# Kernel tuning notes

Measured on AMD Instinct MI355X. Metric: run time of the kernel, lower is better.

## Reference

```python
import jax, jax.numpy as jnp
import numpy as np

D_MODEL = 1024
NUM_HEADS = 16
D_K = D_MODEL // NUM_HEADS


def setup_inputs() -> dict:
    key = jax.random.key(0)
    ks = jax.random.split(key, 9)
    B, T = 2, 2048
    s = 1.0 / np.sqrt(D_MODEL)
    return {
        "x": jax.random.normal(ks[0], (B, T, D_MODEL), dtype=jnp.float32),
        "w_q": jax.random.normal(ks[1], (D_MODEL, D_MODEL), dtype=jnp.float32) * s,
        "b_q": jnp.zeros((D_MODEL,), dtype=jnp.float32),
        "w_k": jax.random.normal(ks[2], (D_MODEL, D_MODEL), dtype=jnp.float32) * s,
        "b_k": jnp.zeros((D_MODEL,), dtype=jnp.float32),
        "w_v": jax.random.normal(ks[3], (D_MODEL, D_MODEL), dtype=jnp.float32) * s,
        "b_v": jnp.zeros((D_MODEL,), dtype=jnp.float32),
        "w_o": jax.random.normal(ks[4], (D_MODEL, D_MODEL), dtype=jnp.float32) * s,
        "b_o": jnp.zeros((D_MODEL,), dtype=jnp.float32),
    }


def reference(x, w_q, b_q, w_k, b_k, w_v, b_v, w_o, b_o):
    B, T, D = x.shape
    H, dk = NUM_HEADS, D_K

    def proj(w, b):
        # [B,T,D] -> [B,H,T,dk]; Linear uses y = x @ W^T + b
        y = jnp.einsum("btd,ed->bte", x, w) + b
        return y.reshape(B, T, H, dk).transpose(0, 2, 1, 3)

    q = proj(w_q, b_q)
    k = proj(w_k, b_k)
    v = proj(w_v, b_v)

    scores = jnp.einsum("bhtd,bhsd->bhts", q, k) / jnp.sqrt(jnp.float32(dk))
    attn = jax.nn.softmax(scores, axis=-1)  # dropout is identity in eval
    out = jnp.einsum("bhts,bhsd->bhtd", attn, v)
    out = out.transpose(0, 2, 1, 3).reshape(B, T, D)
    return jnp.einsum("btd,ed->bte", out, w_o) + b_o
```

## Files before the change

### kernel.cpp

```cpp
#include <hip/hip_runtime.h>

typedef __bf16 bf16x8 __attribute__((ext_vector_type(8)));
typedef float f32x4 __attribute__((ext_vector_type(4)));
typedef float f32x16 __attribute__((ext_vector_type(16)));

__device__ __forceinline__ unsigned short f2bf(float f) {
    unsigned u = __builtin_bit_cast(unsigned, f);
    u += 0x7FFFu + ((u >> 16) & 1u);
    return (unsigned short)(u >> 16);
}
__device__ __forceinline__ float bf2f(unsigned short u) {
    return __builtin_bit_cast(float, (unsigned)u << 16);
}
__device__ __forceinline__ unsigned cvtpk_bf16(float lo, float hi) {
    unsigned r;
    asm("v_cvt_pk_bf16_f32 %0, %1, %2" : "=v"(r) : "v"(lo), "v"(hi));
    return r;
}
__device__ __forceinline__ float exp2_hw(float x) {
    float r;
    asm("v_exp_f32 %0, %1" : "=v"(r) : "v"(x));
    return r;
}

__device__ __forceinline__ void gload16(const void* g, void* l) {
    __builtin_amdgcn_global_load_lds(
        (const __attribute__((address_space(1))) void*)g,
        (__attribute__((address_space(3))) void*)l, 16, 0, 0);
}

__global__ __launch_bounds__(256) void cvt_all(const float* __restrict__ x,
    const float* __restrict__ w0, const float* __restrict__ w1,
    const float* __restrict__ w2, const float* __restrict__ w3,
    unsigned short* __restrict__ xb, unsigned short* __restrict__ wout)
{
    int i = blockIdx.x * 256 + threadIdx.x;
    const float* src;
    unsigned short* dst;
    int j;
    if (i < 1048576) {
        src = x; dst = xb; j = i;
    } else {
        int k = i - 1048576;
        int m = k >> 18;
        src = (m == 0) ? w0 : (m == 1) ? w1 : (m == 2) ? w2 : w3;
        dst = wout + (size_t)m * 1048576;
        j = k & 262143;
    }
    float4 v = reinterpret_cast<const float4*>(src)[j];
    ushort4 o;
    o.x = f2bf(v.x); o.y = f2bf(v.y); o.z = f2bf(v.z); o.w = f2bf(v.w);
    reinterpret_cast<ushort4*>(dst)[j] = o;
}

__global__ __launch_bounds__(256) void qkv_gemm(const unsigned short* __restrict__ X,
    const unsigned short* __restrict__ Wqkv,
    const float* __restrict__ bq, const float* __restrict__ bk, const float* __restrict__ bv,
    unsigned short* __restrict__ Qb, unsigned short* __restrict__ Kb, unsigned short* __restrict__ Vt)
{
    __shared__ __align__(16) unsigned short sA[128 * 64];
    __shared__ __align__(16) unsigned short sW[64 * 64];
    f32x4 acc[4][2] = {};
    const int id = blockIdx.x;
    const int xcd = id & 7, local = id >> 3;
    const int m = (xcd & 1) * 16 + (local & 15);
    const int n = (xcd >> 1) * 12 + (local >> 4);
    const int m0 = m * 128, n0 = n * 64;

    const int tid  = threadIdx.x;
    const int lane = tid & 63;
    const int wv   = tid >> 6;
    const int wm   = wv >> 1, wn = wv & 1;
    const int lrow = lane >> 3;
    const int lchunk = (lane & 7) ^ lrow;

    char* sAc = reinterpret_cast<char*>(sA);
    char* sWc = reinterpret_cast<char*>(sW);

    for (int kt = 0; kt < 1024; kt += 64) {
        __syncthreads();
        #pragma unroll
        for (int j = 0; j < 4; ++j) {
            int row = (wv * 4 + j) * 8 + lrow;
            gload16(X + (size_t)(m0 + row) * 1024 + kt + lchunk * 8, sAc + (wv * 4 + j) * 1024);
        }
        #pragma unroll
        for (int j = 0; j < 2; ++j) {
            int row = (wv * 2 + j) * 8 + lrow;
            gload16(Wqkv + (size_t)(n0 + row) * 1024 + kt + lchunk * 8, sWc + (wv * 2 + j) * 1024);
        }
        __syncthreads();
        #pragma unroll
        for (int kk = 0; kk < 2; ++kk) {
            bf16x8 af[4], wf[2];
            #pragma unroll
            for (int r = 0; r < 4; ++r) {
                int rowA = wm * 64 + r * 16 + (lane & 15);
                int ca = ((kk * 4 + (lane >> 4)) ^ (rowA & 7)) * 16;
                af[r] = *reinterpret_cast<const bf16x8*>(sAc + rowA * 128 + ca);
            }
            #pragma unroll
            for (int c = 0; c < 2; ++c) {
                int rowW = wn * 32 + c * 16 + (lane & 15);
                int cw = ((kk * 4 + (lane >> 4)) ^ (rowW & 7)) * 16;
                wf[c] = *reinterpret_cast<const bf16x8*>(sWc + rowW * 128 + cw);
            }
            #pragma unroll
            for (int r = 0; r < 4; ++r)
                #pragma unroll
                for (int c = 0; c < 2; ++c)
                    acc[r][c] = __builtin_amdgcn_mfma_f32_16x16x32_bf16(af[r], wf[c], acc[r][c], 0, 0, 0);
        }
    }

    const int mid = n0 >> 10;
    const float* bias = (mid == 0) ? bq : (mid == 1) ? bk : bv;
    const float qs = (mid == 0) ? 0.18033688011112042f : 1.0f;
    #pragma unroll
    for (int r = 0; r < 4; ++r) {
        #pragma unroll
        for (int c = 0; c < 2; ++c) {
            int colg = n0 + wn * 32 + c * 16 + (lane & 15);
            int col = colg & 1023;
            float bb = bias[col];
            int row0 = m0 + wm * 64 + r * 16 + 4 * (lane >> 4);
            if (mid == 2) {
                ushort4 sv;
                sv.x = f2bf(acc[r][c][0] + bb);
                sv.y = f2bf(acc[r][c][1] + bb);
                sv.z = f2bf(acc[r][c][2] + bb);
                sv.w = f2bf(acc[r][c][3] + bb);
                *reinterpret_cast<ushort4*>(
                    Vt + ((size_t)((row0 >> 11) * 1024 + col)) * 2048 + (row0 & 2047)) = sv;
            } else {
                #pragma unroll
                for (int e = 0; e < 4; ++e) {
                    unsigned short bf = f2bf((acc[r][c][e] + bb) * qs);
                    if (mid == 0) Qb[(size_t)(row0 + e) * 1024 + col] = bf;
                    else          Kb[(size_t)(row0 + e) * 1024 + col] = bf;
                }
            }
        }
    }
}

__global__ __launch_bounds__(256) void out_gemm(const unsigned short* __restrict__ O,
    const unsigned short* __restrict__ Wo, const float* __restrict__ bo,
    float* __restrict__ out)
{
    __shared__ __align__(16) unsigned short sA[128 * 64];
    __shared__ __align__(16) unsigned short sW[64 * 64];
    f32x4 acc[4][2] = {};
    const int m0 = blockIdx.x * 128, n0 = blockIdx.y * 64;

    const int tid  = threadIdx.x;
    const int lane = tid & 63;
    const int wv   = tid >> 6;
    const int wm   = wv >> 1, wn = wv & 1;
    const int lrow = lane >> 3;
    const int lchunk = (lane & 7) ^ lrow;

    char* sAc = reinterpret_cast<char*>(sA);
    char* sWc = reinterpret_cast<char*>(sW);

    for (int kt = 0; kt < 1024; kt += 64) {
        __syncthreads();
        #pragma unroll
        for (int j = 0; j < 4; ++j) {
            int row = (wv * 4 + j) * 8 + lrow;
            gload16(O + (size_t)(m0 + row) * 1024 + kt + lchunk * 8, sAc + (wv * 4 + j) * 1024);
        }
        #pragma unroll
        for (int j = 0; j < 2; ++j) {
            int row = (wv * 2 + j) * 8 + lrow;
            gload16(Wo + (size_t)(n0 + row) * 1024 + kt + lchunk * 8, sWc + (wv * 2 + j) * 1024);
        }
        __syncthreads();
        #pragma unroll
        for (int kk = 0; kk < 2; ++kk) {
            bf16x8 af[4], wf[2];
            #pragma unroll
            for (int r = 0; r < 4; ++r) {
                int rowA = wm * 64 + r * 16 + (lane & 15);
                int ca = ((kk * 4 + (lane >> 4)) ^ (rowA & 7)) * 16;
                af[r] = *reinterpret_cast<const bf16x8*>(sAc + rowA * 128 + ca);
            }
            #pragma unroll
            for (int c = 0; c < 2; ++c) {
                int rowW = wn * 32 + c * 16 + (lane & 15);
                int cw = ((kk * 4 + (lane >> 4)) ^ (rowW & 7)) * 16;
                wf[c] = *reinterpret_cast<const bf16x8*>(sWc + rowW * 128 + cw);
            }
            #pragma unroll
            for (int r = 0; r < 4; ++r)
                #pragma unroll
                for (int c = 0; c < 2; ++c)
                    acc[r][c] = __builtin_amdgcn_mfma_f32_16x16x32_bf16(af[r], wf[c], acc[r][c], 0, 0, 0);
        }
    }

    #pragma unroll
    for (int r = 0; r < 4; ++r) {
        #pragma unroll
        for (int c = 0; c < 2; ++c) {
            int col = n0 + wn * 32 + c * 16 + (lane & 15);
            float bb = bo[col];
            #pragma unroll
            for (int e = 0; e < 4; ++e) {
                int row = m0 + wm * 64 + r * 16 + 4 * (lane >> 4) + e;
                out[(size_t)row * 1024 + col] = acc[r][c][e] + bb;
            }
        }
    }
}

__global__ __launch_bounds__(256) void combine_kernel(
    const unsigned short* __restrict__ O0, const unsigned short* __restrict__ O1,
    const float* __restrict__ lbase, unsigned short* __restrict__ Ob)
{
    int idx = blockIdx.x * 256 + threadIdx.x;
    int row = idx >> 7;
    int h = (idx & 127) >> 3;
    float lsum = lbase[row * 16 + h] + lbase[65536 + row * 16 + h];
    float inv = 1.0f / lsum;
    uint4 x0 = reinterpret_cast<const uint4*>(O0)[idx];
    uint4 x1 = reinterpret_cast<const uint4*>(O1)[idx];
    const unsigned* p0 = reinterpret_cast<const unsigned*>(&x0);
    const unsigned* p1 = reinterpret_cast<const unsigned*>(&x1);
    uint4 o;
    unsigned* po = reinterpret_cast<unsigned*>(&o);
    #pragma unroll
    for (int wd = 0; wd < 4; ++wd) {
        float lo = bf2f((unsigned short)(p0[wd] & 0xFFFF)) + bf2f((unsigned short)(p1[wd] & 0xFFFF));
        float hi = bf2f((unsigned short)(p0[wd] >> 16)) + bf2f((unsigned short)(p1[wd] >> 16));
        po[wd] = cvtpk_bf16(lo * inv, hi * inv);
    }
    reinterpret_cast<uint4*>(Ob)[idx] = o;
}

__global__ __launch_bounds__(512) void attn_kernel(const unsigned short* __restrict__ Qb,
    const unsigned short* __restrict__ Kb, const unsigned short* __restrict__ Vt,
    unsigned short* __restrict__ Oq0, unsigned short* __restrict__ Oq1,
    float* __restrict__ lbase)
{
    __shared__ __align__(16) unsigned short sK[2][64 * 64];
    __shared__ __align__(16) unsigned short sV[2][64 * 64];

    const int id = blockIdx.x;
    const int swz = (id & 7) * 64 + (id >> 3);
    const int qt = swz & 7;
    const int bh = (swz >> 3) & 31;
    const int half = swz >> 8;
    const int b = bh >> 4, h = bh & 15;
    const int tid = threadIdx.x, lane = tid & 63, wv = tid >> 6;
    const int qq = lane & 31, hi = lane >> 5;

    unsigned short* Oh = half ? Oq1 : Oq0;
    float* lq = lbase + half * 65536;

    const int qrow0 = b * 2048 + qt * 256 + wv * 32;
    const int kv0 = half * 1024;
    const int ntiles = 16;

    bf16x8 qf[4];
    #pragma unroll
    for (int ks = 0; ks < 4; ++ks)
        qf[ks] = *reinterpret_cast<const bf16x8*>(
            Qb + (size_t)(qrow0 + qq) * 1024 + h * 64 + ks * 16 + hi * 8);

    f32x16 oacc[2] = {};
    float l_sum = 0.f;

    const unsigned short* Kbase = Kb + (size_t)b * 2048 * 1024 + h * 64;
    const unsigned short* Vbase = Vt + (size_t)(bh * 64) * 2048;

    const int lrow = lane >> 3;
    const int lchunk = (lane & 7) ^ lrow;

    char* sKbase = reinterpret_cast<char*>(sK);
    char* sVbase = reinterpret_cast<char*>(sV);

    #define FILL(buf, kvoff)                                                              \
        {                                                                                 \
            int row = wv * 8 + lrow;                                                      \
            gload16(Kbase + (size_t)((kvoff) + row) * 1024 + lchunk * 8,                  \
                    sKbase + (buf) * 8192 + wv * 1024);                                   \
            gload16(Vbase + (size_t)row * 2048 + (kvoff) + lchunk * 8,                    \
                    sVbase + (buf) * 8192 + wv * 1024);                                   \
        }

    FILL(0, kv0)
    __syncthreads();

    for (int t = 0; t < ntiles; ++t) {
        const int cur = t & 1;
        if (t < ntiles - 1) { FILL(cur ^ 1, kv0 + (t + 1) * 64) }

        const char* bK = sKbase + cur * 8192;
        const char* bV = sVbase + cur * 8192;

        f32x16 pacc[2];
        __builtin_amdgcn_s_setprio(1);
        #pragma unroll
        for (int mt = 0; mt < 2; ++mt) {
            f32x16 acc = {};
            int row = mt * 32 + qq;
            #pragma unroll
            for (int ks = 0; ks < 4; ++ks) {
                int c = ((ks * 2 + hi) ^ (row & 7)) * 16;
                bf16x8 kf = *reinterpret_cast<const bf16x8*>(bK + row * 128 + c);
                acc = __builtin_amdgcn_mfma_f32_32x32x16_bf16(kf, qf[ks], acc, 0, 0, 0);
            }
            pacc[mt] = acc;
        }
        __builtin_amdgcn_s_setprio(0);

        float rs0 = 0.f, rs1 = 0.f, rs2 = 0.f, rs3 = 0.f;
        #pragma unroll
        for (int mt = 0; mt < 2; ++mt) {
            #pragma unroll
            for (int r = 0; r < 16; r += 4) {
                float p0 = exp2_hw(pacc[mt][r + 0]);
                float p1 = exp2_hw(pacc[mt][r + 1]);
                float p2 = exp2_hw(pacc[mt][r + 2]);
                float p3 = exp2_hw(pacc[mt][r + 3]);
                pacc[mt][r + 0] = p0; rs0 += p0;
                pacc[mt][r + 1] = p1; rs1 += p1;
                pacc[mt][r + 2] = p2; rs2 += p2;
                pacc[mt][r + 3] = p3; rs3 += p3;
            }
        }
        l_sum += (rs0 + rs1) + (rs2 + rs3);

        __builtin_amdgcn_s_setprio(1);
        #pragma unroll
        for (int mt = 0; mt < 2; ++mt) {
            #pragma unroll
            for (int halfk = 0; halfk < 2; ++halfk) {
                int r0 = halfk * 8;
                unsigned A0 = cvtpk_bf16(pacc[mt][r0 + 0], pacc[mt][r0 + 1]);
                unsigned A1 = cvtpk_bf16(pacc[mt][r0 + 2], pacc[mt][r0 + 3]);
                unsigned B0 = cvtpk_bf16(pacc[mt][r0 + 4], pacc[mt][r0 + 5]);
                unsigned B1 = cvtpk_bf16(pacc[mt][r0 + 6], pacc[mt][r0 + 7]);
                unsigned t0 = hi ? A0 : B0;
                unsigned t1 = hi ? A1 : B1;
                unsigned r0x = (unsigned)__shfl_xor((int)t0, 32);
                unsigned r1x = (unsigned)__shfl_xor((int)t1, 32);
                union { unsigned u[4]; bf16x8 v; } pf;
                pf.u[0] = hi ? r0x : A0;
                pf.u[1] = hi ? r1x : A1;
                pf.u[2] = hi ? B0 : r0x;
                pf.u[3] = hi ? B1 : r1x;
                int ks = mt * 2 + halfk;
                #pragma unroll
                for (int dt = 0; dt < 2; ++dt) {
                    int row = dt * 32 + qq;
                    int c = ((ks * 2 + hi) ^ (row & 7)) * 16;
                    bf16x8 vf = *reinterpret_cast<const bf16x8*>(bV + row * 128 + c);
                    oacc[dt] = __builtin_amdgcn_mfma_f32_32x32x16_bf16(vf, pf.v, oacc[dt], 0, 0, 0);
                }
            }
        }
        __builtin_amdgcn_s_setprio(0);
        __syncthreads();
    }

    #pragma unroll
    for (int dt = 0; dt < 2; ++dt) {
        #pragma unroll
        for (int rg = 0; rg < 4; ++rg) {
            int d0 = dt * 32 + rg * 8 + hi * 4;
            ushort4 stv;
            stv.x = f2bf(oacc[dt][rg * 4 + 0]);
            stv.y = f2bf(oacc[dt][rg * 4 + 1]);
            stv.z = f2bf(oacc[dt][rg * 4 + 2]);
            stv.w = f2bf(oacc[dt][rg * 4 + 3]);
            *reinterpret_cast<ushort4*>(Oh + (size_t)(qrow0 + qq) * 1024 + h * 64 + d0) = stv;
        }
    }
    l_sum = l_sum + __shfl_xor(l_sum, 32);
    if (hi == 0)
        lq[(qrow0 + qq) * 16 + h] = l_sum;
}

extern "C" void kernel_launch(void* const* d_in, const int* in_sizes, int n_in,
                              void* d_out, int out_size, void* d_ws, size_t ws_size,
                              hipStream_t stream)
{
    const float* x  = (const float*)d_in[0];
    const float* wq = (const float*)d_in[1];
    const float* bq = (const float*)d_in[2];
    const float* wk = (const float*)d_in[3];
    const float* bk = (const float*)d_in[4];
    const float* wv = (const float*)d_in[5];
    const float* bv = (const float*)d_in[6];
    const float* wo = (const float*)d_in[7];
    const float* bo = (const float*)d_in[8];
    float* out = (float*)d_out;

    char* ws = (char*)d_ws;
    const size_t MB = 1024 * 1024;
    unsigned short* xb   = (unsigned short*)(ws + 0);
    unsigned short* wqkv = (unsigned short*)(ws + 8 * MB);
    unsigned short* wob  = (unsigned short*)(ws + 14 * MB);
    unsigned short* Qb   = (unsigned short*)(ws + 16 * MB);
    unsigned short* Kb   = (unsigned short*)(ws + 24 * MB);
    unsigned short* Vt   = (unsigned short*)(ws + 32 * MB);
    unsigned short* O0   = (unsigned short*)(ws + 40 * MB);
    unsigned short* O1   = (unsigned short*)(ws + 48 * MB);
    float*          lse0 = (float*)(ws + 56 * MB);
    unsigned short* Ob   = Qb;

    cvt_all<<<8192, 256, 0, stream>>>(x, wq, wk, wv, wo, xb, wqkv);

    qkv_gemm<<<1536, 256, 0, stream>>>(xb, wqkv, bq, bk, bv, Qb, Kb, Vt);
    attn_kernel<<<512, 512, 0, stream>>>(Qb, Kb, Vt, O0, O1, lse0);
    combine_kernel<<<2048, 256, 0, stream>>>(O0, O1, lse0, Ob);
    out_gemm<<<dim3(32, 16), 256, 0, stream>>>(Ob, wob, bo, out);
}
```

Baseline: 114.7 us.

## Software-pipeline QK^T of next tile with softmax and PV of current tile

Restructures the attention loop so the QK^T MFMAs for tile t+1 are issued before the exp/softmax and PV MFMAs of tile t, using two score register buffers and a loop unrolled by two. K loads now run two tiles ahead and V loads one tile ahead, each in separate double buffers. The goal is to overlap the exp work (VALU/transcendental) with matrix work and hide shared-memory latency. It costs another 32 floats of live registers per lane, which may reduce occupancy.

```diff
diff --git a/kernel.cpp b/kernel.cpp
--- a/kernel.cpp
+++ b/kernel.cpp
@@ -260,7 +260,6 @@
 
     const int qrow0 = b * 2048 + qt * 256 + wv * 32;
     const int kv0 = half * 1024;
-    const int ntiles = 16;
 
     bf16x8 qf[4];
     #pragma unroll
@@ -269,6 +268,7 @@
             Qb + (size_t)(qrow0 + qq) * 1024 + h * 64 + ks * 16 + hi * 8);
 
     f32x16 oacc[2] = {};
+    f32x16 pP[2][2];
     float l_sum = 0.f;
 
     const unsigned short* Kbase = Kb + (size_t)b * 2048 * 1024 + h * 64;
@@ -280,89 +280,114 @@
     char* sKbase = reinterpret_cast<char*>(sK);
     char* sVbase = reinterpret_cast<char*>(sV);
 
-    #define FILL(buf, kvoff)                                                              \
-        {                                                                                 \
-            int row = wv * 8 + lrow;                                                      \
-            gload16(Kbase + (size_t)((kvoff) + row) * 1024 + lchunk * 8,                  \
-                    sKbase + (buf) * 8192 + wv * 1024);                                   \
-            gload16(Vbase + (size_t)row * 2048 + (kvoff) + lchunk * 8,                    \
-                    sVbase + (buf) * 8192 + wv * 1024);                                   \
-        }
-
-    FILL(0, kv0)
+    #define FILL_K(buf, kvoff)                                                           \
+        {                                                                                \
+            int row = wv * 8 + lrow;                                                     \
+            gload16(Kbase + (size_t)((kvoff) + row) * 1024 + lchunk * 8,                 \
+                    sKbase + (buf) * 8192 + wv * 1024);                                  \
+        }
+    #define FILL_V(buf, kvoff)                                                           \
+        {                                                                                \
+            int row = wv * 8 + lrow;                                                     \
+            gload16(Vbase + (size_t)row * 2048 + (kvoff) + lchunk * 8,                   \
+                    sVbase + (buf) * 8192 + wv * 1024);                                  \
+        }
+
+    #define QKT(S, tn)                                                                   \
+        {                                                                                \
+            const char* bK = sKbase + ((tn) & 1) * 8192;                                 \
+            __builtin_amdgcn_s_setprio(1);                                               \
+            _Pragma("unroll")                                                            \
+            for (int mt = 0; mt < 2; ++mt) {                                             \
+                f32x16 acc = {};                                                         \
+                int row = mt * 32 + qq;                                                  \
+                _Pragma("unroll")                                                        \
+                for (int ks = 0; ks < 4; ++ks) {                                         \
+                    int c = ((ks * 2 + hi) ^ (row & 7)) * 16;                            \
+                    bf16x8 kf = *reinterpret_cast<const bf16x8*>(bK + row * 128 + c);    \
+                    acc = __builtin_amdgcn_mfma_f32_32x32x16_bf16(kf, qf[ks], acc, 0, 0, 0); \
+                }                                                                        \
+                pP[S][mt] = acc;                                                         \
+            }                                                                            \
+            __builtin_amdgcn_s_setprio(0);                                               \
+        }
+
+    #define SMPV(S, t)                                                                   \
+        {                                                                                \
+            float rs0 = 0.f, rs1 = 0.f, rs2 = 0.f, rs3 = 0.f;                            \
+            _Pragma("unroll")                                                            \
+            for (int mt = 0; mt < 2; ++mt) {                                             \
+                _Pragma("unroll")                                                        \
+                for (int r = 0; r < 16; r += 4) {                                        \
+                    float p0 = exp2_hw(pP[S][mt][r + 0]);                                \
+                    float p1 = exp2_hw(pP[S][mt][r + 1]);                                \
+                    float p2 = exp2_hw(pP[S][mt][r + 2]);                                \
+                    float p3 = exp2_hw(pP[S][mt][r + 3]);                                \
+                    pP[S][mt][r + 0] = p0; rs0 += p0;                                    \
+                    pP[S][mt][r + 1] = p1; rs1 += p1;                                    \
+                    pP[S][mt][r + 2] = p2; rs2 += p2;                                    \
+                    pP[S][mt][r + 3] = p3; rs3 += p3;                                    \
+                }                                                                        \
+            }                                                                            \
+            l_sum += (rs0 + rs1) + (rs2 + rs3);                                          \
+            const char* bV = sVbase + ((t) & 1) * 8192;                                  \
+            __builtin_amdgcn_s_setprio(1);                                               \
+            _Pragma("unroll")                                                            \
+            for (int mt = 0; mt < 2; ++mt) {                                             \
+                _Pragma("unroll")                                                        \
+                for (int halfk = 0; halfk < 2; ++halfk) {                                \
+                    int r0 = halfk * 8;                                                  \
+                    unsigned A0 = cvtpk_bf16(pP[S][mt][r0 + 0], pP[S][mt][r0 + 1]);      \
+                    unsigned A1 = cvtpk_bf16(pP[S][mt][r0 + 2], pP[S][mt][r0 + 3]);      \
+                    unsigned B0 = cvtpk_bf16(pP[S][mt][r0 + 4], pP[S][mt][r0 + 5]);      \
+                    unsigned B1 = cvtpk_bf16(pP[S][mt][r0 + 6], pP[S][mt][r0 + 7]);      \
+                    unsigned t0 = hi ? A0 : B0;                                          \
+                    unsigned t1 = hi ? A1 : B1;                                          \
+                    unsigned r0x = (unsigned)__shfl_xor((int)t0, 32);                    \
+                    unsigned r1x = (unsigned)__shfl_xor((int)t1, 32);                    \
+                    union { unsigned u[4]; bf16x8 v; } pf;                               \
+                    pf.u[0] = hi ? r0x : A0;                                             \
+                    pf.u[1] = hi ? r1x : A1;                                             \
+                    pf.u[2] = hi ? B0 : r0x;                                             \
+                    pf.u[3] = hi ? B1 : r1x;                                             \
+                    int ks = mt * 2 + halfk;                                             \
+                    _Pragma("unroll")                                                    \
+                    for (int dt = 0; dt < 2; ++dt) {                                     \
+                        int row = dt * 32 + qq;                                          \
+                        int c = ((ks * 2 + hi) ^ (row & 7)) * 16;                        \
+                        bf16x8 vf = *reinterpret_cast<const bf16x8*>(bV + row * 128 + c);\
+                        oacc[dt] = __builtin_amdgcn_mfma_f32_32x32x16_bf16(vf, pf.v, oacc[dt], 0, 0, 0); \
+                    }                                                                    \
+                }                                                                        \
+            }                                                                            \
+            __builtin_amdgcn_s_setprio(0);                                               \
+        }
+
+    FILL_K(0, kv0)
+    FILL_V(0, kv0)
     __syncthreads();
-
-    for (int t = 0; t < ntiles; ++t) {
-        const int cur = t & 1;
-        if (t < ntiles - 1) { FILL(cur ^ 1, kv0 + (t + 1) * 64) }
-
-        const char* bK = sKbase + cur * 8192;
-        const char* bV = sVbase + cur * 8192;
-
-        f32x16 pacc[2];
-        __builtin_amdgcn_s_setprio(1);
-        #pragma unroll
-        for (int mt = 0; mt < 2; ++mt) {
-            f32x16 acc = {};
-            int row = mt * 32 + qq;
-            #pragma unroll
-            for (int ks = 0; ks < 4; ++ks) {
-                int c = ((ks * 2 + hi) ^ (row & 7)) * 16;
-                bf16x8 kf = *reinterpret_cast<const bf16x8*>(bK + row * 128 + c);
-                acc = __builtin_amdgcn_mfma_f32_32x32x16_bf16(kf, qf[ks], acc, 0, 0, 0);
-            }
-            pacc[mt] = acc;
-        }
-        __builtin_amdgcn_s_setprio(0);
-
-        float rs0 = 0.f, rs1 = 0.f, rs2 = 0.f, rs3 = 0.f;
-        #pragma unroll
-        for (int mt = 0; mt < 2; ++mt) {
-            #pragma unroll
-            for (int r = 0; r < 16; r += 4) {
-                float p0 = exp2_hw(pacc[mt][r + 0]);
-                float p1 = exp2_hw(pacc[mt][r + 1]);
-                float p2 = exp2_hw(pacc[mt][r + 2]);
-                float p3 = exp2_hw(pacc[mt][r + 3]);
-                pacc[mt][r + 0] = p0; rs0 += p0;
-                pacc[mt][r + 1] = p1; rs1 += p1;
-                pacc[mt][r + 2] = p2; rs2 += p2;
-                pacc[mt][r + 3] = p3; rs3 += p3;
-            }
-        }
-        l_sum += (rs0 + rs1) + (rs2 + rs3);
-
-        __builtin_amdgcn_s_setprio(1);
-        #pragma unroll
-        for (int mt = 0; mt < 2; ++mt) {
-            #pragma unroll
-            for (int halfk = 0; halfk < 2; ++halfk) {
-                int r0 = halfk * 8;
-                unsigned A0 = cvtpk_bf16(pacc[mt][r0 + 0], pacc[mt][r0 + 1]);
-                unsigned A1 = cvtpk_bf16(pacc[mt][r0 + 2], pacc[mt][r0 + 3]);
-                unsigned B0 = cvtpk_bf16(pacc[mt][r0 + 4], pacc[mt][r0 + 5]);
-                unsigned B1 = cvtpk_bf16(pacc[mt][r0 + 6], pacc[mt][r0 + 7]);
-                unsigned t0 = hi ? A0 : B0;
-                unsigned t1 = hi ? A1 : B1;
-                unsigned r0x = (unsigned)__shfl_xor((int)t0, 32);
-                unsigned r1x = (unsigned)__shfl_xor((int)t1, 32);
-                union { unsigned u[4]; bf16x8 v; } pf;
-                pf.u[0] = hi ? r0x : A0;
-                pf.u[1] = hi ? r1x : A1;
-                pf.u[2] = hi ? B0 : r0x;
-                pf.u[3] = hi ? B1 : r1x;
-                int ks = mt * 2 + halfk;
-                #pragma unroll
-                for (int dt = 0; dt < 2; ++dt) {
-                    int row = dt * 32 + qq;
-                    int c = ((ks * 2 + hi) ^ (row & 7)) * 16;
-                    bf16x8 vf = *reinterpret_cast<const bf16x8*>(bV + row * 128 + c);
-                    oacc[dt] = __builtin_amdgcn_mfma_f32_32x32x16_bf16(vf, pf.v, oacc[dt], 0, 0, 0);
-                }
-            }
-        }
-        __builtin_amdgcn_s_setprio(0);
+    FILL_K(1, kv0 + 64)
+    QKT(0, 0)
+    __syncthreads();
+
+    for (int tt = 0; tt < 16; tt += 2) {
+        if (tt < 14) FILL_K(tt & 1, kv0 + (tt + 2) * 64)
+        if (tt < 15) {
+            FILL_V((tt + 1) & 1, kv0 + (tt + 1) * 64)
+            QKT(1, tt + 1)
+        }
+        SMPV(0, tt)
         __syncthreads();
+        {
+            const int t1 = tt + 1;
+            if (t1 < 14) FILL_K(t1 & 1, kv0 + (t1 + 2) * 64)
+            if (t1 < 15) {
+                FILL_V((t1 + 1) & 1, kv0 + (t1 + 1) * 64)
+                QKT(0, t1 + 1)
+            }
+            SMPV(1, t1)
+            __syncthreads();
+        }
     }
 
     #pragma unroll
```

New measurement: 122.9 us. 1.07x slower.
